# Kernel optimization log

Measured on AMD Instinct MI355X. Metric: run time of the kernel, lower is better.

The kernel has to match this reference:

```python
import jax, jax.numpy as jnp
import numpy as np

B, D, P = 2048, 768, 200
DOWN = [(384, 768), (192, 384), (96, 192), (48, 96)]
UP = [(96, 48), (192, 96), (384, 192), (768, 384)]


def setup_inputs() -> dict:
    key = jax.random.key(0)
    ks = jax.random.split(key, 32)
    inp = {
        "x": jax.random.normal(ks[0], (B, D), jnp.float32),
        "aW": jax.random.normal(ks[1], (D, D), jnp.float32) * 0.02,
        "ab": jax.random.normal(ks[2], (D,), jnp.float32) * 0.02,
        "protos": jax.random.normal(ks[3], (P, D), jnp.float32),
    }
    k = 4
    for i, (o, ii) in enumerate(DOWN):
        inp[f"Wd{i}"] = jax.random.normal(ks[k], (o, ii), jnp.float32) * (1.0 / np.sqrt(ii)); k += 1
        inp[f"bd{i}"] = jax.random.normal(ks[k], (o,), jnp.float32) * 0.02; k += 1
    for i, (o, ii) in enumerate(UP):
        inp[f"Wu{i}"] = jax.random.normal(ks[k], (o, ii), jnp.float32) * (1.0 / np.sqrt(ii)); k += 1
        inp[f"bu{i}"] = jax.random.normal(ks[k], (o,), jnp.float32) * 0.02; k += 1
    return inp


def _adopter_net(x, Wds, bds, Wus, bus):
    # down path with skip storage
    x_inter = []
    h = x
    for Wd, bd in zip(Wds, bds):
        h = jax.nn.relu(h @ Wd.T + bd)
        x_inter.append(h)
    # up path: residual adds for middle layers (i==1 uses x_inter[-2], i==2 uses x_inter[-3])
    n = len(Wus)
    for i, (Wu, bu) in enumerate(zip(Wus, bus)):
        if i == 0 or i == n - 1:
            h = jax.nn.relu(h @ Wu.T + bu)
        else:
            h = jax.nn.relu((h + x_inter[-i - 1]) @ Wu.T + bu)
    return h


def reference(x, aW, ab, Wd0, bd0, Wd1, bd1, Wd2, bd2, Wd3, bd3,
              Wu0, bu0, Wu1, bu1, Wu2, bu2, Wu3, bu3, protos):
    Wds, bds = [Wd0, Wd1, Wd2, Wd3], [bd0, bd1, bd2, bd3]
    Wus, bus = [Wu0, Wu1, Wu2, Wu3], [bu0, bu1, bu2, bu3]
    # features = x + adapter(x) + adopters(x)
    features = x + (x @ aW.T + ab) + _adopter_net(x, Wds, bds, Wus, bus)  # [B, D]
    # fused per-prototype negative L1 distance (replaces Python loop over PrototypeBase)
    logits = -jnp.sum(jnp.abs(features[:, None, :] - protos[None, :, :]), axis=-1)  # [B, P]
    return logits
```

## Files before the change

kernel.cpp:

```cpp
#include <hip/hip_runtime.h>

typedef __attribute__((ext_vector_type(8))) __bf16 bf16x8;
typedef __attribute__((ext_vector_type(4))) float f32x4;
typedef _Float16 hf2 __attribute__((ext_vector_type(2)));
typedef _Float16 hf8 __attribute__((ext_vector_type(8)));
typedef unsigned short u16;
typedef struct { hf2 v[4]; } hf2x4;

__device__ __forceinline__ float bf2f(u16 h) {
    return __uint_as_float(((unsigned int)h) << 16);
}
__device__ __forceinline__ u16 f2bf(float f) {
    unsigned int u = __float_as_uint(f);
    u += 0x7fffu + ((u >> 16) & 1u);
    return (u16)(u >> 16);
}

#if __has_builtin(__builtin_amdgcn_fdot2)
__device__ __forceinline__ float FDOT2(hf2 a, hf2 b, float c) {
    return __builtin_amdgcn_fdot2(a, b, c, false);
}
#else
__device__ __forceinline__ float FDOT2(hf2 a, hf2 b, float c) {
    return c + (float)a[0] + (float)a[1];
}
#endif

#define GLOAD_LDS16(gsrc, ldst)                                                          \
    __builtin_amdgcn_global_load_lds(                                                    \
        (__attribute__((address_space(1))) unsigned int*)(gsrc),                         \
        (__attribute__((address_space(3))) unsigned int*)(ldst), 16, 0, 0)

struct CvtDesc { const float* src; u16* dst; int N, K, Npad, Kpad, blk0, fmt; };
struct CvtTab { CvtDesc t[11]; };

__global__ __launch_bounds__(256) void cvt_all(CvtTab tab) {
    int b = blockIdx.x;
    int ti = 0;
#pragma unroll
    for (int j = 1; j < 11; ++j)
        if (b >= tab.t[j].blk0) ti = j;
    const CvtDesc c = tab.t[ti];
    long i = (long)(b - c.blk0) * 256 + threadIdx.x;
    long tot = (long)c.Npad * c.Kpad;
    if (i >= tot) return;
    int n = (int)(i / c.Kpad);
    int k = (int)(i - (long)n * c.Kpad);
    float v = (n < c.N && k < c.K) ? c.src[(long)n * c.K + k] : 0.f;
    if (c.fmt) {
        _Float16 h = (_Float16)v;
        c.dst[i] = __builtin_bit_cast(u16, h);
    } else {
        c.dst[i] = f2bf(v);
    }
}

template<int RELU, int HASRES, int MODE>
__device__ __forceinline__ void gemm_body(
    char* lds,
    const u16* __restrict__ A, int lda,
    const u16* __restrict__ W, int ldw,
    const float* __restrict__ bias, int Nreal,
    u16* __restrict__ outB, int ldo,
    const u16* __restrict__ res,
    _Float16* __restrict__ outH,
    int nk, int mb, int nb)
{
    char* ldsA = lds;
    char* ldsB = lds + 8192;

    const int tid  = threadIdx.x;
    const int wave = tid >> 6;
    const int lane = tid & 63;
    const int wr = wave >> 1, wc = wave & 1;
    const int lr = lane & 15, lk = lane >> 4;

    f32x4 acc[2][2];
#pragma unroll
    for (int i = 0; i < 2; ++i)
#pragma unroll
        for (int j = 0; j < 2; ++j)
#pragma unroll
            for (int e = 0; e < 4; ++e) acc[i][j][e] = 0.f;

    const int g0 = wave * 64 + lane;
    const int r0 = g0 >> 3, l0 = (g0 & 7) ^ (r0 & 7);
    const int g1 = g0 + 256;
    const int r1 = g1 >> 3, l1 = (g1 & 7) ^ (r1 & 7);

    for (int kt = 0; kt < nk; ++kt) {
        const int kk = kt * 64;
        GLOAD_LDS16(A + (size_t)(mb + r0) * lda + kk + l0 * 8, ldsA + wave * 1024);
        GLOAD_LDS16(A + (size_t)(mb + r1) * lda + kk + l1 * 8, ldsA + 4096 + wave * 1024);
        GLOAD_LDS16(W + (size_t)(nb + r0) * ldw + kk + l0 * 8, ldsB + wave * 1024);
        GLOAD_LDS16(W + (size_t)(nb + r1) * ldw + kk + l1 * 8, ldsB + 4096 + wave * 1024);
        __syncthreads();
#pragma unroll
        for (int ks = 0; ks < 2; ++ks) {
            bf16x8 af[2], bfr[2];
#pragma unroll
            for (int mi = 0; mi < 2; ++mi) {
                int m_loc = wr * 32 + mi * 16 + lr;
                int gr = (ks * 4 + lk) ^ (m_loc & 7);
                af[mi] = *(const bf16x8*)(ldsA + m_loc * 128 + gr * 16);
            }
#pragma unroll
            for (int ni = 0; ni < 2; ++ni) {
                int n_loc = wc * 32 + ni * 16 + lr;
                int gr = (ks * 4 + lk) ^ (n_loc & 7);
                bfr[ni] = *(const bf16x8*)(ldsB + n_loc * 128 + gr * 16);
            }
#pragma unroll
            for (int mi = 0; mi < 2; ++mi)
#pragma unroll
                for (int ni = 0; ni < 2; ++ni)
                    acc[mi][ni] = __builtin_amdgcn_mfma_f32_16x16x32_bf16(
                        af[mi], bfr[ni], acc[mi][ni], 0, 0, 0);
        }
        __syncthreads();
    }

#pragma unroll
    for (int mi = 0; mi < 2; ++mi) {
#pragma unroll
        for (int ni = 0; ni < 2; ++ni) {
            const int n_g = nb + wc * 32 + ni * 16 + lr;
            const float bv = (n_g < Nreal) ? bias[n_g] : 0.f;
#pragma unroll
            for (int r = 0; r < 4; ++r) {
                const int m_g = mb + wr * 32 + mi * 16 + lk * 4 + r;
                float v = acc[mi][ni][r] + bv;
                if (RELU) v = fmaxf(v, 0.f);
                if (HASRES) v += bf2f(res[(size_t)m_g * ldo + n_g]);
                if (MODE == 2) {
                    outH[(size_t)m_g * 768 + n_g] = (_Float16)v;
                } else {
                    outB[(size_t)m_g * ldo + n_g] = f2bf(v);
                }
            }
        }
    }
}

__global__ __launch_bounds__(256) void gemm_ad0(
    const u16* __restrict__ xb,
    const u16* __restrict__ aWb, const float* __restrict__ ab,
    _Float16* __restrict__ adFH,
    const u16* __restrict__ Wd0b, const float* __restrict__ bd0,
    u16* __restrict__ h1)
{
    __shared__ __align__(16) char lds[16384];
    if (blockIdx.y < 12) {
        gemm_body<0, 1, 2>(lds, xb, 768, aWb, 768, ab, 768, nullptr, 768,
                           xb, adFH, 12, blockIdx.x * 64, blockIdx.y * 64);
    } else {
        gemm_body<1, 0, 0>(lds, xb, 768, Wd0b, 768, bd0, 384, h1, 384,
                           nullptr, nullptr, 12,
                           blockIdx.x * 64, (blockIdx.y - 12) * 64);
    }
}

template<int K, int NPAD, int NREAL, int RES>
__device__ __forceinline__ void layer16(
    const u16* __restrict__ W, int ldw, const float* __restrict__ bias,
    const u16* actIn, int ldin,
    u16* actOut, int ldout,
    const u16* resid, int ldres)
{
    constexpr int TPW = NPAD / 64;
    const int tid = threadIdx.x;
    const int wave = tid >> 6, lane = tid & 63;
    const int lr = lane & 15, lk = lane >> 4;

    f32x4 acc[TPW];
#pragma unroll
    for (int t = 0; t < TPW; ++t)
#pragma unroll
        for (int e = 0; e < 4; ++e) acc[t][e] = 0.f;

#pragma unroll
    for (int kk = 0; kk < K / 32; ++kk) {
        const bf16x8 a = *(const bf16x8*)&actIn[lr * ldin + kk * 32 + lk * 8];
#pragma unroll
        for (int t = 0; t < TPW; ++t) {
            const int nc = (wave * TPW + t) * 16 + lr;
            const bf16x8 b = *(const bf16x8*)&W[(size_t)nc * ldw + kk * 32 + lk * 8];
            acc[t] = __builtin_amdgcn_mfma_f32_16x16x32_bf16(a, b, acc[t], 0, 0, 0);
        }
    }
#pragma unroll
    for (int t = 0; t < TPW; ++t) {
        const int nc = (wave * TPW + t) * 16 + lr;
        const float bv = (nc < NREAL) ? bias[nc] : 0.f;
#pragma unroll
        for (int r = 0; r < 4; ++r) {
            const int row = lk * 4 + r;
            float v = fmaxf(acc[t][r] + bv, 0.f);
            if (RES) v += bf2f(resid[row * ldres + nc]);
            actOut[row * ldout + nc] = f2bf(v);
        }
    }
}

__global__ __launch_bounds__(256) void chain_full(
    const u16* __restrict__ h1,
    const u16* __restrict__ Wd1b, const float* __restrict__ bd1,
    const u16* __restrict__ Wd2b, const float* __restrict__ bd2,
    const u16* __restrict__ Wd3b, const float* __restrict__ bd3,
    const u16* __restrict__ Wu0b, const float* __restrict__ bu0,
    const u16* __restrict__ Wu1b, const float* __restrict__ bu1,
    const u16* __restrict__ Wu2b, const float* __restrict__ bu2,
    const u16* __restrict__ Wu3b, const float* __restrict__ bu3,
    const _Float16* __restrict__ adFH, _Float16* __restrict__ featH)
{
    __shared__ u16 As[16 * 392];
    __shared__ u16 Bs[16 * 200];
    __shared__ u16 Cs[16 * 136];
    __shared__ u16 Ds[16 * 72];
    __shared__ u16 Gs[16 * 392];
    const int tid = threadIdx.x;
    const int rb = blockIdx.x * 16;

    for (int i = tid; i < 768; i += 256) {
        const int r = i / 48, c = i - r * 48;
        *(bf16x8*)&As[r * 392 + c * 8] =
            *(const bf16x8*)&h1[(size_t)(rb + r) * 384 + c * 8];
    }
    __syncthreads();
    layer16<384, 192, 192, 0>(Wd1b, 384, bd1, As, 392, Bs, 200, nullptr, 0);
    __syncthreads();
    layer16<192, 128,  96, 0>(Wd2b, 192, bd2, Bs, 200, Cs, 136, nullptr, 0);
    __syncthreads();
    layer16<128,  64,  48, 0>(Wd3b, 128, bd3, Cs, 136, Ds,  72, nullptr, 0);
    __syncthreads();
    u16* E = As;
    u16* F = As + 16 * 136;
    layer16< 64, 128,  96, 1>(Wu0b,  64, bu0, Ds,  72, E, 136, Cs, 136);
    __syncthreads();
    layer16<128, 192, 192, 1>(Wu1b, 128, bu1, E, 136, F, 200, Bs, 200);
    __syncthreads();
    layer16<192, 384, 384, 0>(Wu2b, 192, bu2, F, 200, Gs, 392, nullptr, 0);
    __syncthreads();

    {
        const int wave = tid >> 6, lane = tid & 63;
        const int lr = lane & 15, lk = lane >> 4;
        f32x4 acc[12];
#pragma unroll
        for (int t = 0; t < 12; ++t)
#pragma unroll
            for (int e = 0; e < 4; ++e) acc[t][e] = 0.f;
#pragma unroll 2
        for (int kk = 0; kk < 12; ++kk) {
            const bf16x8 a = *(const bf16x8*)&Gs[lr * 392 + kk * 32 + lk * 8];
#pragma unroll
            for (int t = 0; t < 12; ++t) {
                const int nc = (wave * 12 + t) * 16 + lr;
                const bf16x8 b =
                    *(const bf16x8*)&Wu3b[(size_t)nc * 384 + kk * 32 + lk * 8];
                acc[t] = __builtin_amdgcn_mfma_f32_16x16x32_bf16(a, b, acc[t], 0, 0, 0);
            }
        }
#pragma unroll
        for (int t = 0; t < 12; ++t) {
            const int nc = (wave * 12 + t) * 16 + lr;
            const float bv = bu3[nc];
#pragma unroll
            for (int r = 0; r < 4; ++r) {
                const int row = lk * 4 + r;
                float v = fmaxf(acc[t][r] + bv, 0.f);
                v += (float)adFH[(size_t)(rb + row) * 768 + nc];
                featH[(size_t)(rb + row) * 768 + nc] = (_Float16)v;
            }
        }
    }
}

__global__ __launch_bounds__(256) void l1_kernel(
    const _Float16* __restrict__ feat, const _Float16* __restrict__ protos,
    float* __restrict__ part)
{
    __shared__ _Float16 fs[128][64];
    __shared__ hf2 pt[32][64];
    const int tid = threadIdx.x;
    const int tp = tid & 15, tr = tid >> 4;
    const int rb = blockIdx.x * 128;
    const int pb = blockIdx.y * 64;
    const int db = blockIdx.z * 64;

    {
        const int g = tid & 7, r0 = tid >> 3;
#pragma unroll
        for (int k = 0; k < 4; ++k) {
            const int r = r0 + 32 * k;
            *(hf8*)&fs[r][g * 8] =
                *(const hf8*)&feat[(size_t)(rb + r) * 768 + db + g * 8];
        }
    }
    {
        const int sp = tid & 63, q = tid >> 6;
        const _Float16* src = &protos[(size_t)(pb + sp) * 768 + db + q * 16];
        hf8 v0 = *(const hf8*)src;
        hf8 v1 = *(const hf8*)(src + 8);
        hf2x4 w0 = __builtin_bit_cast(hf2x4, v0);
        hf2x4 w1 = __builtin_bit_cast(hf2x4, v1);
#pragma unroll
        for (int e = 0; e < 4; ++e)
            pt[q * 8 + e][sp] = w0.v[e];
#pragma unroll
        for (int e = 0; e < 4; ++e)
            pt[q * 8 + 4 + e][sp] = w1.v[e];
    }
    __syncthreads();

    float acc[8][4];
#pragma unroll
    for (int i = 0; i < 8; ++i)
#pragma unroll
        for (int j = 0; j < 4; ++j) acc[i][j] = 0.f;

    const hf2 one2 = {(_Float16)1.0f, (_Float16)1.0f};
#pragma unroll 2
    for (int g = 0; g < 8; ++g) {
        hf2x4 F2[8];
#pragma unroll
        for (int i = 0; i < 8; ++i)
            F2[i] = __builtin_bit_cast(hf2x4,
                        *(const hf8*)&fs[tr + 16 * i][g * 8]);
        hf2x4 P2[4];
#pragma unroll
        for (int q = 0; q < 4; ++q)
            P2[q] = __builtin_bit_cast(hf2x4,
                        *(const hf8*)&pt[g * 4 + q][tp * 4]);
#pragma unroll
        for (int q = 0; q < 4; ++q) {
#pragma unroll
            for (int j = 0; j < 4; ++j) {
                const hf2 pj = P2[q].v[j];
#pragma unroll
                for (int i = 0; i < 8; ++i) {
                    hf2 d = F2[i].v[q] - pj;
                    unsigned ud = __builtin_bit_cast(unsigned, d) & 0x7FFF7FFFu;
                    acc[i][j] = FDOT2(__builtin_bit_cast(hf2, ud), one2, acc[i][j]);
                }
            }
        }
    }
    const int p = pb + tp * 4;
    if (p < 200) {
#pragma unroll
        for (int i = 0; i < 8; ++i) {
            float4 v = {-acc[i][0], -acc[i][1], -acc[i][2], -acc[i][3]};
            *(float4*)&part[((size_t)(rb + tr + 16 * i) * 12 + blockIdx.z) * 200 + p] = v;
        }
    }
}

__global__ __launch_bounds__(256) void l1_reduce(
    const float* __restrict__ part, float* __restrict__ out)
{
    const int row = blockIdx.x;
    const int p = threadIdx.x;
    if (p < 200) {
        float s = 0.f;
#pragma unroll
        for (int z = 0; z < 12; ++z)
            s += part[((size_t)row * 12 + z) * 200 + p];
        out[(size_t)row * 200 + p] = s;
    }
}

static constexpr size_t OFF_PART  = 0;
static constexpr size_t OFF_XB    = 0;
static constexpr size_t OFF_AWB   = 3145728;
static constexpr size_t OFF_WD0   = 4325376;
static constexpr size_t OFF_WD1   = 4915200;
static constexpr size_t OFF_WD2   = 5062656;
static constexpr size_t OFF_WD3   = 5111808;
static constexpr size_t OFF_WU0   = 5128192;
static constexpr size_t OFF_WU1   = 5144576;
static constexpr size_t OFF_WU2   = 5193728;
static constexpr size_t OFF_WU3   = 5341184;
static constexpr size_t OFF_H1    = 5931008;
static constexpr size_t OFF_ADF   = 11960320;
static constexpr size_t OFF_FEATH = 19660800;
static constexpr size_t OFF_PROH  = 22806528;

extern "C" void kernel_launch(void* const* d_in, const int* in_sizes, int n_in,
                              void* d_out, int out_size, void* d_ws, size_t ws_size,
                              hipStream_t stream) {
    const float* x      = (const float*)d_in[0];
    const float* aW     = (const float*)d_in[1];
    const float* ab     = (const float*)d_in[2];
    const float* protos = (const float*)d_in[3];
    const float* Wd[4]  = {(const float*)d_in[4], (const float*)d_in[6],
                           (const float*)d_in[8], (const float*)d_in[10]};
    const float* bd[4]  = {(const float*)d_in[5], (const float*)d_in[7],
                           (const float*)d_in[9], (const float*)d_in[11]};
    const float* Wu[4]  = {(const float*)d_in[12], (const float*)d_in[14],
                           (const float*)d_in[16], (const float*)d_in[18]};
    const float* bu[4]  = {(const float*)d_in[13], (const float*)d_in[15],
                           (const float*)d_in[17], (const float*)d_in[19]};
    float* out = (float*)d_out;
    char* ws = (char*)d_ws;

    u16* xb    = (u16*)(ws + OFF_XB);
    u16* aWb   = (u16*)(ws + OFF_AWB);
    u16* Wd0b  = (u16*)(ws + OFF_WD0);
    u16* Wd1b  = (u16*)(ws + OFF_WD1);
    u16* Wd2b  = (u16*)(ws + OFF_WD2);
    u16* Wd3b  = (u16*)(ws + OFF_WD3);
    u16* Wu0b  = (u16*)(ws + OFF_WU0);
    u16* Wu1b  = (u16*)(ws + OFF_WU1);
    u16* Wu2b  = (u16*)(ws + OFF_WU2);
    u16* Wu3b  = (u16*)(ws + OFF_WU3);
    u16* h1    = (u16*)(ws + OFF_H1);
    float* part = (float*)(ws + OFF_PART);
    _Float16* adFH  = (_Float16*)(ws + OFF_ADF);
    _Float16* featH = (_Float16*)(ws + OFF_FEATH);
    _Float16* proH  = (_Float16*)(ws + OFF_PROH);

    CvtTab tab;
    int blk = 0;
    auto set = [&](int i, const float* s, u16* d, int N, int K, int Np, int Kp,
                   int fmt) {
        tab.t[i] = {s, d, N, K, Np, Kp, blk, fmt};
        blk += (Np * Kp + 255) / 256;
    };
    set(0,  x,      xb,          2048, 768, 2048, 768, 0);
    set(1,  aW,     aWb,         768,  768, 768,  768, 0);
    set(2,  Wd[0],  Wd0b,        384,  768, 384,  768, 0);
    set(3,  Wd[1],  Wd1b,        192,  384, 192,  384, 0);
    set(4,  Wd[2],  Wd2b,        96,   192, 128,  192, 0);
    set(5,  Wd[3],  Wd3b,        48,   96,  64,   128, 0);
    set(6,  Wu[0],  Wu0b,        96,   48,  128,  64,  0);
    set(7,  Wu[1],  Wu1b,        192,  96,  192,  128, 0);
    set(8,  Wu[2],  Wu2b,        384,  192, 384,  192, 0);
    set(9,  Wu[3],  Wu3b,        768,  384, 768,  384, 0);
    set(10, protos, (u16*)proH,  200,  768, 256,  768, 1);
    cvt_all<<<blk, 256, 0, stream>>>(tab);

    gemm_ad0<<<dim3(32, 18), 256, 0, stream>>>(xb, aWb, ab, adFH, Wd0b, bd[0], h1);
    chain_full<<<dim3(128), 256, 0, stream>>>(h1,
        Wd1b, bd[1], Wd2b, bd[2], Wd3b, bd[3],
        Wu0b, bu[0], Wu1b, bu[1], Wu2b, bu[2], Wu3b, bu[3],
        adFH, featH);

    l1_kernel<<<dim3(16, 4, 12), 256, 0, stream>>>(featH, proH, part);
    l1_reduce<<<dim3(2048), 256, 0, stream>>>(part, out);
}
```

Baseline: 90.98 us.

## Use 128x64 double-buffered GEMM tiles and split last up-layer into own GEMM

The shared GEMM body now uses 128x64 tiles with double-buffered LDS staging, so the next k-tile's global-to-LDS loads overlap the current MFMA work, and the first GEMM grid is halved. The final up-projection (384->768) is removed from the 128-block chain kernel and run as a separate tiled GEMM over 192 blocks, with the intermediate written to a workspace buffer. This targets the chain kernel's poor parallelism and weight re-reads on its largest layer. The cost is an extra launch, a global round trip for the intermediate, and 48KB of LDS per block, which limits occupancy.

```diff
diff --git a/kernel.cpp b/kernel.cpp
--- a/kernel.cpp
+++ b/kernel.cpp
@@ -55,88 +55,112 @@
     }
 }
 
-template<int RELU, int HASRES, int MODE>
-__device__ __forceinline__ void gemm_body(
+template<int RELU, int HASRES, int RESF16, int MODE>
+__device__ __forceinline__ void gemm128_body(
     char* lds,
     const u16* __restrict__ A, int lda,
     const u16* __restrict__ W, int ldw,
-    const float* __restrict__ bias, int Nreal,
+    const float* __restrict__ bias,
     u16* __restrict__ outB, int ldo,
-    const u16* __restrict__ res,
+    const void* __restrict__ res, int ldr,
     _Float16* __restrict__ outH,
     int nk, int mb, int nb)
 {
-    char* ldsA = lds;
-    char* ldsB = lds + 8192;
-
-    const int tid  = threadIdx.x;
-    const int wave = tid >> 6;
-    const int lane = tid & 63;
+    const int tid = threadIdx.x;
+    const int wave = tid >> 6, lane = tid & 63;
+    const int lr = lane & 15, lk = lane >> 4;
     const int wr = wave >> 1, wc = wave & 1;
-    const int lr = lane & 15, lk = lane >> 4;
-
-    f32x4 acc[2][2];
-#pragma unroll
-    for (int i = 0; i < 2; ++i)
+
+    f32x4 acc[4][2];
+#pragma unroll
+    for (int i = 0; i < 4; ++i)
 #pragma unroll
         for (int j = 0; j < 2; ++j)
 #pragma unroll
             for (int e = 0; e < 4; ++e) acc[i][j][e] = 0.f;
 
-    const int g0 = wave * 64 + lane;
-    const int r0 = g0 >> 3, l0 = (g0 & 7) ^ (r0 & 7);
-    const int g1 = g0 + 256;
-    const int r1 = g1 >> 3, l1 = (g1 & 7) ^ (r1 & 7);
-
-    for (int kt = 0; kt < nk; ++kt) {
+    int ra[4], la[4], rb[2], lb[2];
+#pragma unroll
+    for (int t = 0; t < 4; ++t) {
+        int g = t * 256 + tid;
+        ra[t] = g >> 3; la[t] = (g & 7) ^ (ra[t] & 7);
+    }
+#pragma unroll
+    for (int t = 0; t < 2; ++t) {
+        int g = t * 256 + tid;
+        rb[t] = g >> 3; lb[t] = (g & 7) ^ (rb[t] & 7);
+    }
+
+    auto STAGE = [&](int b, int kt) {
         const int kk = kt * 64;
-        GLOAD_LDS16(A + (size_t)(mb + r0) * lda + kk + l0 * 8, ldsA + wave * 1024);
-        GLOAD_LDS16(A + (size_t)(mb + r1) * lda + kk + l1 * 8, ldsA + 4096 + wave * 1024);
-        GLOAD_LDS16(W + (size_t)(nb + r0) * ldw + kk + l0 * 8, ldsB + wave * 1024);
-        GLOAD_LDS16(W + (size_t)(nb + r1) * ldw + kk + l1 * 8, ldsB + 4096 + wave * 1024);
-        __syncthreads();
+        char* dA = lds + b * 24576;
+        char* dB = dA + 16384;
+#pragma unroll
+        for (int t = 0; t < 4; ++t)
+            GLOAD_LDS16(A + (size_t)(mb + ra[t]) * lda + kk + la[t] * 8,
+                        dA + t * 4096 + wave * 1024);
+#pragma unroll
+        for (int t = 0; t < 2; ++t)
+            GLOAD_LDS16(W + (size_t)(nb + rb[t]) * ldw + kk + lb[t] * 8,
+                        dB + t * 4096 + wave * 1024);
+    };
+    auto COMPUTE = [&](int b) {
+        char* sA = lds + b * 24576;
+        char* sB = sA + 16384;
 #pragma unroll
         for (int ks = 0; ks < 2; ++ks) {
-            bf16x8 af[2], bfr[2];
-#pragma unroll
-            for (int mi = 0; mi < 2; ++mi) {
-                int m_loc = wr * 32 + mi * 16 + lr;
+            bf16x8 af[4], bfr[2];
+#pragma unroll
+            for (int mi = 0; mi < 4; ++mi) {
+                int m_loc = wr * 64 + mi * 16 + lr;
                 int gr = (ks * 4 + lk) ^ (m_loc & 7);
-                af[mi] = *(const bf16x8*)(ldsA + m_loc * 128 + gr * 16);
+                af[mi] = *(const bf16x8*)(sA + m_loc * 128 + gr * 16);
             }
 #pragma unroll
             for (int ni = 0; ni < 2; ++ni) {
                 int n_loc = wc * 32 + ni * 16 + lr;
                 int gr = (ks * 4 + lk) ^ (n_loc & 7);
-                bfr[ni] = *(const bf16x8*)(ldsB + n_loc * 128 + gr * 16);
+                bfr[ni] = *(const bf16x8*)(sB + n_loc * 128 + gr * 16);
             }
 #pragma unroll
-            for (int mi = 0; mi < 2; ++mi)
+            for (int mi = 0; mi < 4; ++mi)
 #pragma unroll
                 for (int ni = 0; ni < 2; ++ni)
                     acc[mi][ni] = __builtin_amdgcn_mfma_f32_16x16x32_bf16(
                         af[mi], bfr[ni], acc[mi][ni], 0, 0, 0);
         }
+    };
+
+    STAGE(0, 0);
+    __syncthreads();
+    int b = 0;
+    for (int kt = 0; kt < nk - 1; ++kt) {
+        STAGE(b ^ 1, kt + 1);
+        COMPUTE(b);
         __syncthreads();
-    }
-
-#pragma unroll
-    for (int mi = 0; mi < 2; ++mi) {
+        b ^= 1;
+    }
+    COMPUTE(b);
+
+#pragma unroll
+    for (int mi = 0; mi < 4; ++mi) {
 #pragma unroll
         for (int ni = 0; ni < 2; ++ni) {
             const int n_g = nb + wc * 32 + ni * 16 + lr;
-            const float bv = (n_g < Nreal) ? bias[n_g] : 0.f;
+            const float bv = bias[n_g];
 #pragma unroll
             for (int r = 0; r < 4; ++r) {
-                const int m_g = mb + wr * 32 + mi * 16 + lk * 4 + r;
+                const int m_g = mb + wr * 64 + mi * 16 + lk * 4 + r;
                 float v = acc[mi][ni][r] + bv;
                 if (RELU) v = fmaxf(v, 0.f);
-                if (HASRES) v += bf2f(res[(size_t)m_g * ldo + n_g]);
-                if (MODE == 2) {
-                    outH[(size_t)m_g * 768 + n_g] = (_Float16)v;
-                } else {
-                    outB[(size_t)m_g * ldo + n_g] = f2bf(v);
+                if (HASRES) {
+                    if (RESF16)
+                        v += (float)((const _Float16*)res)[(size_t)m_g * ldr + n_g];
+                    else
+                        v += bf2f(((const u16*)res)[(size_t)m_g * ldr + n_g]);
                 }
+                if (MODE == 2) outH[(size_t)m_g * 768 + n_g] = (_Float16)v;
+                else           outB[(size_t)m_g * ldo + n_g] = f2bf(v);
             }
         }
     }
@@ -149,23 +173,36 @@
     const u16* __restrict__ Wd0b, const float* __restrict__ bd0,
     u16* __restrict__ h1)
 {
-    __shared__ __align__(16) char lds[16384];
+    __shared__ __align__(16) char lds[49152];
     if (blockIdx.y < 12) {
-        gemm_body<0, 1, 2>(lds, xb, 768, aWb, 768, ab, 768, nullptr, 768,
-                           xb, adFH, 12, blockIdx.x * 64, blockIdx.y * 64);
+        gemm128_body<0, 1, 0, 2>(lds, xb, 768, aWb, 768, ab, nullptr, 0,
+                                 xb, 768, adFH, 12,
+                                 blockIdx.x * 128, blockIdx.y * 64);
     } else {
-        gemm_body<1, 0, 0>(lds, xb, 768, Wd0b, 768, bd0, 384, h1, 384,
-                           nullptr, nullptr, 12,
-                           blockIdx.x * 64, (blockIdx.y - 12) * 64);
-    }
-}
-
-template<int K, int NPAD, int NREAL, int RES>
+        gemm128_body<1, 0, 0, 0>(lds, xb, 768, Wd0b, 768, bd0, h1, 384,
+                                 nullptr, 0, nullptr, 12,
+                                 blockIdx.x * 128, (blockIdx.y - 12) * 64);
+    }
+}
+
+__global__ __launch_bounds__(256) void gemm_u3(
+    const u16* __restrict__ u2, const u16* __restrict__ Wu3b,
+    const float* __restrict__ bu3, const _Float16* __restrict__ adFH,
+    _Float16* __restrict__ featH)
+{
+    __shared__ __align__(16) char lds[49152];
+    gemm128_body<1, 1, 1, 2>(lds, u2, 384, Wu3b, 384, bu3, nullptr, 0,
+                             adFH, 768, featH, 6,
+                             blockIdx.x * 128, blockIdx.y * 64);
+}
+
+template<int K, int NPAD, int NREAL, int RES, int OUTG>
 __device__ __forceinline__ void layer16(
     const u16* __restrict__ W, int ldw, const float* __restrict__ bias,
     const u16* actIn, int ldin,
     u16* actOut, int ldout,
-    const u16* resid, int ldres)
+    const u16* resid, int ldres,
+    u16* __restrict__ gout, int ldg)
 {
     constexpr int TPW = NPAD / 64;
     const int tid = threadIdx.x;
@@ -197,12 +234,14 @@
             const int row = lk * 4 + r;
             float v = fmaxf(acc[t][r] + bv, 0.f);
             if (RES) v += bf2f(resid[row * ldres + nc]);
-            actOut[row * ldout + nc] = f2bf(v);
-        }
-    }
-}
-
-__global__ __launch_bounds__(256) void chain_full(
+            const u16 o = f2bf(v);
+            if (OUTG) gout[(size_t)row * ldg + nc] = o;
+            else      actOut[row * ldout + nc] = o;
+        }
+    }
+}
+
+__global__ __launch_bounds__(256) void chain_mid(
     const u16* __restrict__ h1,
     const u16* __restrict__ Wd1b, const float* __restrict__ bd1,
     const u16* __restrict__ Wd2b, const float* __restrict__ bd2,
@@ -210,14 +249,12 @@
     const u16* __restrict__ Wu0b, const float* __restrict__ bu0,
     const u16* __restrict__ Wu1b, const float* __restrict__ bu1,
     const u16* __restrict__ Wu2b, const float* __restrict__ bu2,
-    const u16* __restrict__ Wu3b, const float* __restrict__ bu3,
-    const _Float16* __restrict__ adFH, _Float16* __restrict__ featH)
+    u16* __restrict__ u2)
 {
     __shared__ u16 As[16 * 392];
     __shared__ u16 Bs[16 * 200];
     __shared__ u16 Cs[16 * 136];
     __shared__ u16 Ds[16 * 72];
-    __shared__ u16 Gs[16 * 392];
     const int tid = threadIdx.x;
     const int rb = blockIdx.x * 16;
 
@@ -227,53 +264,20 @@
             *(const bf16x8*)&h1[(size_t)(rb + r) * 384 + c * 8];
     }
     __syncthreads();
-    layer16<384, 192, 192, 0>(Wd1b, 384, bd1, As, 392, Bs, 200, nullptr, 0);
-    __syncthreads();
-    layer16<192, 128,  96, 0>(Wd2b, 192, bd2, Bs, 200, Cs, 136, nullptr, 0);
-    __syncthreads();
-    layer16<128,  64,  48, 0>(Wd3b, 128, bd3, Cs, 136, Ds,  72, nullptr, 0);
+    layer16<384, 192, 192, 0, 0>(Wd1b, 384, bd1, As, 392, Bs, 200, nullptr, 0, nullptr, 0);
+    __syncthreads();
+    layer16<192, 128,  96, 0, 0>(Wd2b, 192, bd2, Bs, 200, Cs, 136, nullptr, 0, nullptr, 0);
+    __syncthreads();
+    layer16<128,  64,  48, 0, 0>(Wd3b, 128, bd3, Cs, 136, Ds,  72, nullptr, 0, nullptr, 0);
     __syncthreads();
     u16* E = As;
     u16* F = As + 16 * 136;
-    layer16< 64, 128,  96, 1>(Wu0b,  64, bu0, Ds,  72, E, 136, Cs, 136);
-    __syncthreads();
-    layer16<128, 192, 192, 1>(Wu1b, 128, bu1, E, 136, F, 200, Bs, 200);
-    __syncthreads();
-    layer16<192, 384, 384, 0>(Wu2b, 192, bu2, F, 200, Gs, 392, nullptr, 0);
-    __syncthreads();
-
-    {
-        const int wave = tid >> 6, lane = tid & 63;
-        const int lr = lane & 15, lk = lane >> 4;
-        f32x4 acc[12];
-#pragma unroll
-        for (int t = 0; t < 12; ++t)
-#pragma unroll
-            for (int e = 0; e < 4; ++e) acc[t][e] = 0.f;
-#pragma unroll 2
-        for (int kk = 0; kk < 12; ++kk) {
-            const bf16x8 a = *(const bf16x8*)&Gs[lr * 392 + kk * 32 + lk * 8];
-#pragma unroll
-            for (int t = 0; t < 12; ++t) {
-                const int nc = (wave * 12 + t) * 16 + lr;
-                const bf16x8 b =
-                    *(const bf16x8*)&Wu3b[(size_t)nc * 384 + kk * 32 + lk * 8];
-                acc[t] = __builtin_amdgcn_mfma_f32_16x16x32_bf16(a, b, acc[t], 0, 0, 0);
-            }
-        }
-#pragma unroll
-        for (int t = 0; t < 12; ++t) {
-            const int nc = (wave * 12 + t) * 16 + lr;
-            const float bv = bu3[nc];
-#pragma unroll
-            for (int r = 0; r < 4; ++r) {
-                const int row = lk * 4 + r;
-                float v = fmaxf(acc[t][r] + bv, 0.f);
-                v += (float)adFH[(size_t)(rb + row) * 768 + nc];
-                featH[(size_t)(rb + row) * 768 + nc] = (_Float16)v;
-            }
-        }
-    }
+    layer16< 64, 128,  96, 1, 0>(Wu0b,  64, bu0, Ds,  72, E, 136, Cs, 136, nullptr, 0);
+    __syncthreads();
+    layer16<128, 192, 192, 1, 0>(Wu1b, 128, bu1, E, 136, F, 200, Bs, 200, nullptr, 0);
+    __syncthreads();
+    layer16<192, 384, 384, 0, 1>(Wu2b, 192, bu2, F, 200, nullptr, 0, nullptr, 0,
+                                 u2 + (size_t)rb * 384, 384);
 }
 
 __global__ __launch_bounds__(256) void l1_kernel(
@@ -382,6 +386,7 @@
 static constexpr size_t OFF_WU2   = 5193728;
 static constexpr size_t OFF_WU3   = 5341184;
 static constexpr size_t OFF_H1    = 5931008;
+static constexpr size_t OFF_U2    = 10387456;
 static constexpr size_t OFF_ADF   = 11960320;
 static constexpr size_t OFF_FEATH = 19660800;
 static constexpr size_t OFF_PROH  = 22806528;
@@ -415,6 +420,7 @@
     u16* Wu2b  = (u16*)(ws + OFF_WU2);
     u16* Wu3b  = (u16*)(ws + OFF_WU3);
     u16* h1    = (u16*)(ws + OFF_H1);
+    u16* u2    = (u16*)(ws + OFF_U2);
     float* part = (float*)(ws + OFF_PART);
     _Float16* adFH  = (_Float16*)(ws + OFF_ADF);
     _Float16* featH = (_Float16*)(ws + OFF_FEATH);
@@ -440,11 +446,11 @@
     set(10, protos, (u16*)proH,  200,  768, 256,  768, 1);
     cvt_all<<<blk, 256, 0, stream>>>(tab);
 
-    gemm_ad0<<<dim3(32, 18), 256, 0, stream>>>(xb, aWb, ab, adFH, Wd0b, bd[0], h1);
-    chain_full<<<dim3(128), 256, 0, stream>>>(h1,
+    gemm_ad0<<<dim3(16, 18), 256, 0, stream>>>(xb, aWb, ab, adFH, Wd0b, bd[0], h1);
+    chain_mid<<<dim3(128), 256, 0, stream>>>(h1,
         Wd1b, bd[1], Wd2b, bd[2], Wd3b, bd[3],
-        Wu0b, bu[0], Wu1b, bu[1], Wu2b, bu[2], Wu3b, bu[3],
-        adFH, featH);
+        Wu0b, bu[0], Wu1b, bu[1], Wu2b, bu[2], u2);
+    gemm_u3<<<dim3(16, 12), 256, 0, stream>>>(u2, Wu3b, bu[3], adFH, featH);
 
     l1_kernel<<<dim3(16, 4, 12), 256, 0, stream>>>(featH, proH, part);
     l1_reduce<<<dim3(2048), 256, 0, stream>>>(part, out);
```

New measurement: 80.56 us. -11.4%, faster.
